# Performance work log

Measured on AMD Instinct MI355X. Metric: run time of the kernel, lower is better.

The kernel has to match this reference:

```python
import jax, jax.numpy as jnp
import numpy as np

NUM_GRAPHS = 1024  # static number of segments for global_mean_pool


def setup_inputs() -> dict:
    key = jax.random.key(0)
    ks = jax.random.split(key, 16)
    N, E, F_IN, H = 100000, 1000000, 32, 64
    NUM_ATOM, NUM_ACT, L = 16, 8, 3
    s = 0.05
    x = jax.random.normal(ks[0], (N, F_IN), dtype=jnp.float32)
    edge_index = jax.random.randint(ks[1], (2, E), 0, N, dtype=jnp.int64)
    batch = jnp.sort(jax.random.randint(ks[2], (N,), 0, NUM_GRAPHS, dtype=jnp.int64))
    W_emb = jax.random.normal(ks[3], (F_IN, H), dtype=jnp.float32) * s
    b_emb = jnp.zeros((H,), dtype=jnp.float32)
    W_convs = jax.random.normal(ks[4], (L, H, H), dtype=jnp.float32) * s
    b_convs = jnp.zeros((L, H), dtype=jnp.float32)
    W_act = jax.random.normal(ks[5], (H, NUM_ACT), dtype=jnp.float32) * s
    b_act = jnp.zeros((NUM_ACT,), dtype=jnp.float32)
    W_tgt = jax.random.normal(ks[6], (H, 1), dtype=jnp.float32) * s
    b_tgt = jnp.zeros((1,), dtype=jnp.float32)
    W_atom = jax.random.normal(ks[7], (H, NUM_ATOM), dtype=jnp.float32) * s
    b_atom = jnp.zeros((NUM_ATOM,), dtype=jnp.float32)
    return {"x": x, "edge_index": edge_index, "batch": batch,
            "W_emb": W_emb, "b_emb": b_emb, "W_convs": W_convs, "b_convs": b_convs,
            "W_act": W_act, "b_act": b_act, "W_tgt": W_tgt, "b_tgt": b_tgt,
            "W_atom": W_atom, "b_atom": b_atom}


def reference(x, edge_index, batch, W_emb, b_emb, W_convs, b_convs,
              W_act, b_act, W_tgt, b_tgt, W_atom, b_atom):
    N = x.shape[0]
    # --- GCN normalization with self-loops (PyG GCNConv default) ---
    self_idx = jnp.arange(N, dtype=edge_index.dtype)
    src = jnp.concatenate([edge_index[0], self_idx])  # message source (row)
    dst = jnp.concatenate([edge_index[1], self_idx])  # aggregation target (col)
    ones_e = jnp.ones(src.shape[0], dtype=x.dtype)
    deg = jax.ops.segment_sum(ones_e, dst, num_segments=N)  # in-degree + self-loop
    dinv = jnp.where(deg > 0, jax.lax.rsqrt(deg), 0.0)
    norm = (dinv[src] * dinv[dst])[:, None]  # [E+N, 1]

    h = jax.nn.relu(x @ W_emb + b_emb)  # node embedding
    for i in range(W_convs.shape[0]):
        m = (h @ W_convs[i])[src] * norm            # gather + scale
        agg = jax.ops.segment_sum(m, dst, num_segments=N)  # scatter-add
        h = jax.nn.relu(agg + b_convs[i])

    # --- global mean pool over graphs ---
    cnt = jax.ops.segment_sum(jnp.ones(N, dtype=x.dtype), batch, num_segments=NUM_GRAPHS)
    pooled = jax.ops.segment_sum(h, batch, num_segments=NUM_GRAPHS)
    pooled = pooled / jnp.maximum(cnt, 1.0)[:, None]

    action_type_logits = pooled @ W_act + b_act            # [G, num_action_types]
    target_node_logits = (h @ W_tgt + b_tgt)[:, 0]         # [N]
    new_atom_type_logits = pooled @ W_atom + b_atom        # [G, num_atom_types]
    return (action_type_logits, target_node_logits, new_atom_type_logits, h)
```

## Files before the change

kernel.cpp:

```cpp
#include <hip/hip_runtime.h>
#include <hip/hip_fp16.h>

#define HD 64
#define FIN 32
#define NG 1024
#define STRIDE 64
#define SLOT0 4
#define DEGCAP 59
#define SH 72

#define BINW 128
#define NBMAX 1024
#define EPB 8192
#define BINCAP 2048

typedef _Float16 f16x8 __attribute__((ext_vector_type(8)));
typedef float f32x4 __attribute__((ext_vector_type(4)));
typedef int i32x4 __attribute__((ext_vector_type(4)));

__device__ __forceinline__ int fmap(int jt, int c) {
    return (jt < 2) ? (2 * c + jt) : (32 + 2 * c + (jt - 2));
}

__global__ __launch_bounds__(256) void k_prep(const int* __restrict__ dst,
                                              int* __restrict__ blkHist,
                                              int E, int NBINS,
                                              __half2* __restrict__ BaZR,
                                              __half2* __restrict__ BbZR,
                                              const float* __restrict__ Wconv,
                                              __half* __restrict__ Wf, int wtotal,
                                              const float* __restrict__ Wemb,
                                              __half* __restrict__ Wef) {
    __shared__ int hist[NBMAX];
    int b = blockIdx.x, t = threadIdx.x;
    if (b < 48) {
        int tid = b * 256 + t;
        if (tid < wtotal) {
            int layer = tid >> 12;
            int r = tid & 4095;
            int frag = r >> 9, lane = (r >> 3) & 63, e = r & 7;
            int jt = frag >> 1, kh = frag & 1;
            int k = kh * 32 + (lane >> 4) * 8 + e;
            int n = fmap(jt, lane & 15);
            Wf[tid] = (_Float16)Wconv[(size_t)layer * 4096 + k * 64 + n];
        }
    } else if (b < 56) {
        int tid = (b - 48) * 256 + t;
        if (tid < 2048) {
            int jt = tid >> 9, lane = (tid >> 3) & 63, e = tid & 7;
            int k = (lane >> 4) * 8 + e;
            int n = fmap(jt, lane & 15);
            Wef[tid] = (_Float16)Wemb[k * HD + n];
        }
    } else if (b == 56) {
        __half2 z = __floats2half2_rn(0.f, 0.f);
        if (t < 32) BaZR[t] = z;
        else if (t < 64) BbZR[t - 32] = z;
    }
    int e0 = b * EPB;
    if (e0 < E) {
        for (int i = t; i < NBMAX; i += 256) hist[i] = 0;
        __syncthreads();
        int e1 = e0 + EPB; if (e1 > E) e1 = E;
        for (int e = e0 + t; e < e1; e += 256) atomicAdd(&hist[dst[e] >> 7], 1);
        __syncthreads();
        for (int i = t; i < NBINS; i += 256) blkHist[b * NBMAX + i] = hist[i];
    }
}

__global__ __launch_bounds__(256) void k_scanA(int* __restrict__ blkHist,
                                               int* __restrict__ binTot, int nb) {
    __shared__ int s[256];
    int i = blockIdx.x;
    int t = threadIdx.x;
    int x = (t < nb) ? blkHist[t * NBMAX + i] : 0;
    s[t] = x;
    __syncthreads();
    for (int off = 1; off < 256; off <<= 1) {
        int v = s[t];
        int u = (t >= off) ? s[t - off] : 0;
        __syncthreads();
        s[t] = v + u;
        __syncthreads();
    }
    if (t < nb) blkHist[t * NBMAX + i] = s[t] - x;
    if (t == 255) binTot[i] = s[255];
}

__global__ __launch_bounds__(256) void k_scatter(const int* __restrict__ src,
                                                 const int* __restrict__ dst,
                                                 const int* __restrict__ blkBase,
                                                 int* __restrict__ binned,
                                                 int E, int NBINS) {
    __shared__ int base[NBMAX];
    __shared__ int lpos[NBMAX];
    int b = blockIdx.x, t = threadIdx.x;
    for (int i = t; i < NBMAX; i += 256) {
        lpos[i] = 0;
        base[i] = (i < NBINS) ? blkBase[b * NBMAX + i] : 0;
    }
    __syncthreads();
    int e0 = b * EPB;
    int e1 = e0 + EPB; if (e1 > E) e1 = E;
    for (int e = e0 + t; e < e1; e += 256) {
        int d = dst[e];
        int bin = d >> 7;
        int off = base[bin] + atomicAdd(&lpos[bin], 1);
        if (off < BINCAP)
            binned[bin * BINCAP + off] = (src[e] << 7) | (d & (BINW - 1));
    }
}

__global__ __launch_bounds__(256) void k_csr(const int* __restrict__ binned,
                                             const int* __restrict__ binTot,
                                             int* __restrict__ col, int N) {
    __shared__ int img[BINW * 64];
    __shared__ int cnt[BINW];
    int b = blockIdx.x, t = threadIdx.x;
    for (int i = t; i < BINW; i += 256) cnt[i] = 0;
    __syncthreads();
    int s = b * BINCAP;
    int tot = binTot[b]; if (tot > BINCAP) tot = BINCAP;
    int e = s + tot;
    for (int i = s + t; i < e; i += 256) {
        int w = binned[i];
        int ld = w & (BINW - 1);
        int p = atomicAdd(&cnt[ld], 1);
        if (p < STRIDE - SLOT0) img[ld * 64 + SLOT0 + p] = (int)((unsigned)w >> 7);
    }
    __syncthreads();
    for (int i = t; i < BINW; i += 256) img[i * 64] = cnt[i];
    __syncthreads();
    int v0 = b * BINW;
    int* out = col + ((size_t)v0 << 6);
    for (int j = t; j < BINW * 16; j += 256) {
        int row = j >> 4, j16 = j & 15;
        int node = v0 + row;
        int deg = cnt[row]; if (deg > DEGCAP) deg = DEGCAP;
        bool keep = (j16 == 0) || (j16 <= ((deg + 3) >> 2));
        if (node < N && keep) {
            i32x4 val = *(i32x4*)&img[j * 4];
            __builtin_nontemporal_store(val, (i32x4*)(out + j * 4));
        }
    }
}

__device__ __forceinline__ void gemm_from_lds(const __half* hs, const float* dvs,
                                              const float4* __restrict__ Wf4,
                                              __half2* __restrict__ Bout,
                                              int node0, int N, int t) {
    int lane = t & 63;
    int wv = t >> 6;
    int lm = lane & 15, kq = lane >> 4;
    union U { float4 f; f16x8 h; };
    U a0, a1;
    const __half* hrow = hs + (size_t)(wv * 16 + lm) * SH;
    a0.f = *(const float4*)(hrow + kq * 8);
    a1.f = *(const float4*)(hrow + 32 + kq * 8);
    f32x4 acc[4];
#pragma unroll
    for (int jt = 0; jt < 4; jt++) acc[jt] = (f32x4){0.f, 0.f, 0.f, 0.f};
#pragma unroll
    for (int jt = 0; jt < 4; jt++) {
        U b0, b1;
        b0.f = Wf4[(jt * 2 + 0) * 64 + lane];
        b1.f = Wf4[(jt * 2 + 1) * 64 + lane];
        acc[jt] = __builtin_amdgcn_mfma_f32_16x16x32_f16(a0.h, b0.h, acc[jt], 0, 0, 0);
        acc[jt] = __builtin_amdgcn_mfma_f32_16x16x32_f16(a1.h, b1.h, acc[jt], 0, 0, 0);
    }
#pragma unroll
    for (int r = 0; r < 4; r++) {
        int lv = wv * 16 + kq * 4 + r;
        int v = node0 + lv;
        if (v < N) {
            float dv = dvs[lv];
            *(Bout + (size_t)v * 32 + lm) = __floats2half2_rn(acc[0][r] * dv, acc[1][r] * dv);
            *(Bout + (size_t)v * 32 + 16 + lm) = __floats2half2_rn(acc[2][r] * dv, acc[3][r] * dv);
        }
    }
}

__global__ __launch_bounds__(256) void k_emb_gemm0(const float* __restrict__ x,
                                                   const float4* __restrict__ Wef4,
                                                   const float* __restrict__ bemb,
                                                   const int* __restrict__ col,
                                                   const float4* __restrict__ Wf0,
                                                   __half2* __restrict__ Bout, int N) {
    __shared__ __half hs[64 * SH];
    __shared__ float dvs[64];
    int t = threadIdx.x;
    int lane = t & 63;
    int wv = t >> 6;
    int node0 = blockIdx.x * 64;
    int nodew = node0 + wv * 16;
    int m = lane & 15, kq = lane >> 4;

    int vm = nodew + m;
    if (vm > N - 1) vm = N - 1;
    const float4* xr = (const float4*)(x + (size_t)vm * FIN + kq * 8);
    float4 xa = xr[0], xb = xr[1];
    f16x8 a;
    a[0] = (_Float16)xa.x; a[1] = (_Float16)xa.y; a[2] = (_Float16)xa.z; a[3] = (_Float16)xa.w;
    a[4] = (_Float16)xb.x; a[5] = (_Float16)xb.y; a[6] = (_Float16)xb.z; a[7] = (_Float16)xb.w;

    union U { float4 f; f16x8 h; };
    f32x4 acc[4];
#pragma unroll
    for (int jt = 0; jt < 4; jt++) {
        U b; b.f = Wef4[jt * 64 + lane];
        acc[jt] = (f32x4){0.f, 0.f, 0.f, 0.f};
        acc[jt] = __builtin_amdgcn_mfma_f32_16x16x32_f16(a, b.h, acc[jt], 0, 0, 0);
    }
    float b01x = bemb[2 * m], b01y = bemb[2 * m + 1];
    float b23x = bemb[32 + 2 * m], b23y = bemb[32 + 2 * m + 1];
    __half2 z = __floats2half2_rn(0.f, 0.f);
#pragma unroll
    for (int r = 0; r < 4; r++) {
        int lv = wv * 16 + kq * 4 + r;
        int v = node0 + lv;
        __half2 p01 = z, p23 = z;
        if (v < N) {
            p01 = __floats2half2_rn(fmaxf(acc[0][r] + b01x, 0.f),
                                    fmaxf(acc[1][r] + b01y, 0.f));
            p23 = __floats2half2_rn(fmaxf(acc[2][r] + b23x, 0.f),
                                    fmaxf(acc[3][r] + b23y, 0.f));
        }
        *(__half2*)(hs + (size_t)lv * SH + 2 * m) = p01;
        *(__half2*)(hs + (size_t)lv * SH + 32 + 2 * m) = p23;
        if (m == 0)
            dvs[lv] = (v < N) ? rsqrtf((float)(col[(size_t)v << 6] + 1)) : 1.f;
    }
    __syncthreads();
    gemm_from_lds(hs, dvs, Wf0, Bout, node0, N, t);
}

__global__ __launch_bounds__(256) void k_layer(const __half2* __restrict__ Bin,
                                               const int* __restrict__ col,
                                               const float* __restrict__ bias,
                                               const float4* __restrict__ Wnext,
                                               __half2* __restrict__ Bout,
                                               int N, int ZR) {
    __shared__ __half hs[64 * SH];
    __shared__ float dvs[64];
    int t = threadIdx.x;
    int lane = t & 63;
    int wv = t >> 6;
    int node0 = blockIdx.x * 64;
    int q = lane >> 4, p = lane & 15;
    float4 b4 = *(const float4*)(bias + 4 * p);

#pragma unroll
    for (int pass = 0; pass < 4; pass++) {
        int lv = wv * 16 + pass * 4 + q;
        int v = node0 + lv;
        int vc = (v < N) ? v : 0;
        const int* bucket = col + ((size_t)vc << 6);
        int degraw = bucket[0];
        int deg = degraw > DEGCAP ? DEGCAP : degraw;
        int dmax = deg;
        dmax = max(dmax, __shfl_xor(dmax, 16, 64));
        dmax = max(dmax, __shfl_xor(dmax, 32, 64));
        int rounds = (dmax + 4) >> 2;

        float2 a0 = make_float2(0.f, 0.f), a1 = make_float2(0.f, 0.f);
        for (int rd = 0; rd < rounds; rd++) {
            int4 iq = *(const int4*)(bucket + SLOT0 + rd * 4);
            int idx[4] = {iq.x, iq.y, iq.z, iq.w};
#pragma unroll
            for (int r = 0; r < 4; r++) {
                int i = rd * 4 + r;
                idx[r] = (i < deg) ? idx[r] : ((i == deg) ? vc : ZR);
            }
            float2 raw[4];
#pragma unroll
            for (int r = 0; r < 4; r++)
                raw[r] = *(const float2*)(Bin + (size_t)idx[r] * 32 + p * 2);
#pragma unroll
            for (int r = 0; r < 4; r++) {
                float2 f0 = __half22float2(((const __half2*)&raw[r])[0]);
                float2 f1 = __half22float2(((const __half2*)&raw[r])[1]);
                a0.x += f0.x; a0.y += f0.y; a1.x += f1.x; a1.y += f1.y;
            }
        }
        float dv = rsqrtf((float)(degraw + 1));
        float r0 = fmaxf(dv * a0.x + b4.x, 0.f);
        float r1 = fmaxf(dv * a0.y + b4.y, 0.f);
        float r2 = fmaxf(dv * a1.x + b4.z, 0.f);
        float r3 = fmaxf(dv * a1.y + b4.w, 0.f);
        if (v >= N) { r0 = r1 = r2 = r3 = 0.f; dv = 1.f; }
        __half* hrow = hs + (size_t)lv * SH + 4 * p;
        *(__half2*)(hrow) = __floats2half2_rn(r0, r1);
        *(__half2*)(hrow + 2) = __floats2half2_rn(r2, r3);
        if (p == 0) dvs[lv] = dv;
    }
    __syncthreads();
    gemm_from_lds(hs, dvs, Wnext, Bout, node0, N, t);
}

__global__ __launch_bounds__(256) void k_gather_last(const __half2* __restrict__ Bin,
                                                     const int* __restrict__ col,
                                                     const float* __restrict__ bias,
                                                     float* __restrict__ hout,
                                                     const float* __restrict__ Wtgt,
                                                     const float* __restrict__ btgt,
                                                     float* __restrict__ tgt,
                                                     int N, int ZR) {
    int t = threadIdx.x;
    int lane = t & 63;
    int wv = t >> 6;
    int q = lane >> 4, p = lane & 15;
    int v = blockIdx.x * 16 + wv * 4 + q;
    if (v >= N) return;

    const int* bucket = col + ((size_t)v << 6);
    int degraw = bucket[0];
    int deg = degraw > DEGCAP ? DEGCAP : degraw;
    int dmax = deg;
    dmax = max(dmax, __shfl_xor(dmax, 16, 64));
    dmax = max(dmax, __shfl_xor(dmax, 32, 64));
    int rounds = (dmax + 4) >> 2;

    float2 a0 = make_float2(0.f, 0.f), a1 = make_float2(0.f, 0.f);
    for (int rd = 0; rd < rounds; rd++) {
        int4 iq = *(const int4*)(bucket + SLOT0 + rd * 4);
        int idx[4] = {iq.x, iq.y, iq.z, iq.w};
#pragma unroll
        for (int r = 0; r < 4; r++) {
            int i = rd * 4 + r;
            idx[r] = (i < deg) ? idx[r] : ((i == deg) ? v : ZR);
        }
        float2 raw[4];
#pragma unroll
        for (int r = 0; r < 4; r++)
            raw[r] = *(const float2*)(Bin + (size_t)idx[r] * 32 + p * 2);
#pragma unroll
        for (int r = 0; r < 4; r++) {
            float2 f0 = __half22float2(((const __half2*)&raw[r])[0]);
            float2 f1 = __half22float2(((const __half2*)&raw[r])[1]);
            a0.x += f0.x; a0.y += f0.y; a1.x += f1.x; a1.y += f1.y;
        }
    }
    float dv = rsqrtf((float)(degraw + 1));
    float4 b4 = *(const float4*)(bias + 4 * p);
    float r0 = fmaxf(dv * a0.x + b4.x, 0.f);
    float r1 = fmaxf(dv * a0.y + b4.y, 0.f);
    float r2 = fmaxf(dv * a1.x + b4.z, 0.f);
    float r3 = fmaxf(dv * a1.y + b4.w, 0.f);
    f32x4 o = (f32x4){r0, r1, r2, r3};
    __builtin_nontemporal_store(o, (f32x4*)(hout + (size_t)v * HD + 4 * p));
    float4 w4 = *(const float4*)(Wtgt + 4 * p);
    float pp = r0 * w4.x + r1 * w4.y + r2 * w4.z + r3 * w4.w;
    pp += __shfl_xor(pp, 1, 64); pp += __shfl_xor(pp, 2, 64);
    pp += __shfl_xor(pp, 4, 64); pp += __shfl_xor(pp, 8, 64);
    if (p == 0) __builtin_nontemporal_store(pp + btgt[0], tgt + v);
}

__global__ __launch_bounds__(256) void k_pool(const float* __restrict__ h,
                                              const int* __restrict__ batch,
                                              const float* __restrict__ Wact,
                                              const float* __restrict__ bact,
                                              const float* __restrict__ Watom,
                                              const float* __restrict__ batom,
                                              float* __restrict__ out_act,
                                              float* __restrict__ out_atom, int N) {
    int g = blockIdx.x;
    int t = threadIdx.x;
    int q = t >> 4, p = t & 15;
    int lo = 0, hi = N;
    while (lo < hi) { int mid = (lo + hi) >> 1; if (batch[mid] < g) lo = mid + 1; else hi = mid; }
    int s = lo;
    hi = N;
    while (lo < hi) { int mid = (lo + hi) >> 1; if (batch[mid] < g + 1) lo = mid + 1; else hi = mid; }
    int e2 = lo;
    float4 acc = make_float4(0.f, 0.f, 0.f, 0.f);
    for (int v = s + q; v < e2; v += 16) {
        float4 c = *(const float4*)(h + (size_t)v * HD + p * 4);
        acc.x += c.x; acc.y += c.y; acc.z += c.z; acc.w += c.w;
    }
    __shared__ float4 part[16][16];
    part[q][p] = acc;
    __syncthreads();
    __shared__ float pl[HD];
    if (t < 16) {
        float4 tot = part[0][t];
#pragma unroll
        for (int k = 1; k < 16; k++) {
            float4 c = part[k][t];
            tot.x += c.x; tot.y += c.y; tot.z += c.z; tot.w += c.w;
        }
        float cnt = fmaxf((float)(e2 - s), 1.f);
        pl[t * 4 + 0] = tot.x / cnt; pl[t * 4 + 1] = tot.y / cnt;
        pl[t * 4 + 2] = tot.z / cnt; pl[t * 4 + 3] = tot.w / cnt;
    }
    __syncthreads();
    if (t < 8) {
        float a = bact[t];
#pragma unroll
        for (int k = 0; k < HD; k++) a += pl[k] * Wact[k * 8 + t];
        out_act[g * 8 + t] = a;
    }
    if (t < 16) {
        float a = batom[t];
#pragma unroll
        for (int k = 0; k < HD; k++) a += pl[k] * Watom[k * 16 + t];
        out_atom[g * 16 + t] = a;
    }
}

extern "C" void kernel_launch(void* const* d_in, const int* in_sizes, int n_in,
                              void* d_out, int out_size, void* d_ws, size_t ws_size,
                              hipStream_t stream) {
    const float* x     = (const float*)d_in[0];
    const int*   ei    = (const int*)d_in[1];
    const int*   batch = (const int*)d_in[2];
    const float* Wemb  = (const float*)d_in[3];
    const float* bemb  = (const float*)d_in[4];
    const float* Wconv = (const float*)d_in[5];
    const float* bconv = (const float*)d_in[6];
    const float* Wact  = (const float*)d_in[7];
    const float* bact  = (const float*)d_in[8];
    const float* Wtgt  = (const float*)d_in[9];
    const float* btgt  = (const float*)d_in[10];
    const float* Watom = (const float*)d_in[11];
    const float* batom = (const float*)d_in[12];

    const int N = in_sizes[0] / FIN;
    const int E = in_sizes[1] / 2;
    const int L = in_sizes[5] / (HD * HD);
    const int Npad = (N + 63) & ~63;
    const int ZR = Npad;

    int*     col = (int*)d_ws;
    __half2* Ba  = (__half2*)(col + ((size_t)N << 6));
    __half2* Bb  = Ba + (size_t)(Npad + 64) * 32;
    __half*  Wf  = (__half*)(Bb + (size_t)(Npad + 64) * 32);
    __half*  Wef = Wf + (size_t)L * 4096;

    int* binned  = (int*)Bb;
    int* blkHist = (int*)((char*)Bb + (8u << 20));
    int* binTot  = (int*)((char*)Bb + (9u << 20));

    const int* srcA = ei;
    const int* dstA = ei + E;

    float* out_act  = (float*)d_out;
    float* out_tgt  = out_act + (size_t)NG * 8;
    float* out_atom = out_tgt + N;
    float* out_h    = out_atom + (size_t)NG * 16;

    const int nbG = (N + 63) / 64;
    const int nbLast = (N + 15) / 16;
    const int wtotal = L * 4096;
    const int nbF1 = (E + EPB - 1) / EPB;
    const int NBINS = (N + BINW - 1) / BINW;
    const int nbPrep = nbF1 > 57 ? nbF1 : 57;

    k_prep<<<nbPrep, 256, 0, stream>>>(dstA, blkHist, E, NBINS,
                                       Ba + (size_t)ZR * 32, Bb + (size_t)ZR * 32,
                                       Wconv, Wf, wtotal, Wemb, Wef);
    k_scanA<<<NBINS, 256, 0, stream>>>(blkHist, binTot, nbF1);
    k_scatter<<<nbF1, 256, 0, stream>>>(srcA, dstA, blkHist, binned, E, NBINS);
    k_csr<<<NBINS, 256, 0, stream>>>(binned, binTot, col, N);
    k_emb_gemm0<<<nbG, 256, 0, stream>>>(x, (const float4*)Wef, bemb, col,
                                         (const float4*)Wf, Ba, N);

    __half2* cur = Ba;
    __half2* nxt = Bb;
    for (int l = 0; l < L - 1; ++l) {
        k_layer<<<nbG, 256, 0, stream>>>(cur, col, bconv + l * HD,
                                         (const float4*)(Wf + (size_t)(l + 1) * 4096),
                                         nxt, N, ZR);
        __half2* tmp = cur; cur = nxt; nxt = tmp;
    }
    k_gather_last<<<nbLast, 256, 0, stream>>>(cur, col, bconv + (size_t)(L - 1) * HD,
                                              out_h, Wtgt, btgt, out_tgt, N, ZR);
    k_pool<<<NG, 256, 0, stream>>>(out_h, batch, Wact, bact, Watom, batom,
                                   out_act, out_atom, N);
}
```

Before: 233.8 us.

## Drop the scan kernel by computing bin prefix sums inside scatter and csr

Removes the separate k_scanA launch. k_prep now writes the per-block histogram transposed, k_scatter computes each bin's base offset by summing earlier blocks serially, and k_csr gets each bin total with a shared atomic reduction. This saves one kernel launch and dependency point, at the cost of a serial prefix loop of up to ~123 reads per bin per thread in scatter. It also replaces nontemporal stores with plain stores for the CSR column output and the final h output, which changes how those writes interact with the cache.

Measured after the change: 256.6 us. 1.1x slower.

```diff
diff --git a/kernel.cpp b/kernel.cpp
--- a/kernel.cpp
+++ b/kernel.cpp
@@ -23,7 +23,7 @@
 }
 
 __global__ __launch_bounds__(256) void k_prep(const int* __restrict__ dst,
-                                              int* __restrict__ blkHist,
+                                              int* __restrict__ blkHistT,
                                               int E, int NBINS,
                                               __half2* __restrict__ BaZR,
                                               __half2* __restrict__ BbZR,
@@ -64,32 +64,13 @@
         int e1 = e0 + EPB; if (e1 > E) e1 = E;
         for (int e = e0 + t; e < e1; e += 256) atomicAdd(&hist[dst[e] >> 7], 1);
         __syncthreads();
-        for (int i = t; i < NBINS; i += 256) blkHist[b * NBMAX + i] = hist[i];
-    }
-}
-
-__global__ __launch_bounds__(256) void k_scanA(int* __restrict__ blkHist,
-                                               int* __restrict__ binTot, int nb) {
-    __shared__ int s[256];
-    int i = blockIdx.x;
-    int t = threadIdx.x;
-    int x = (t < nb) ? blkHist[t * NBMAX + i] : 0;
-    s[t] = x;
-    __syncthreads();
-    for (int off = 1; off < 256; off <<= 1) {
-        int v = s[t];
-        int u = (t >= off) ? s[t - off] : 0;
-        __syncthreads();
-        s[t] = v + u;
-        __syncthreads();
-    }
-    if (t < nb) blkHist[t * NBMAX + i] = s[t] - x;
-    if (t == 255) binTot[i] = s[255];
+        for (int i = t; i < NBINS; i += 256) blkHistT[i * 256 + b] = hist[i];
+    }
 }
 
 __global__ __launch_bounds__(256) void k_scatter(const int* __restrict__ src,
                                                  const int* __restrict__ dst,
-                                                 const int* __restrict__ blkBase,
+                                                 const int* __restrict__ blkHistT,
                                                  int* __restrict__ binned,
                                                  int E, int NBINS) {
     __shared__ int base[NBMAX];
@@ -97,7 +78,12 @@
     int b = blockIdx.x, t = threadIdx.x;
     for (int i = t; i < NBMAX; i += 256) {
         lpos[i] = 0;
-        base[i] = (i < NBINS) ? blkBase[b * NBMAX + i] : 0;
+        int s = 0;
+        if (i < NBINS) {
+            const int* row = blkHistT + i * 256;
+            for (int b2 = 0; b2 < b; b2++) s += row[b2];
+        }
+        base[i] = s;
     }
     __syncthreads();
     int e0 = b * EPB;
@@ -112,15 +98,19 @@
 }
 
 __global__ __launch_bounds__(256) void k_csr(const int* __restrict__ binned,
-                                             const int* __restrict__ binTot,
+                                             const int* __restrict__ blkHistT, int nb,
                                              int* __restrict__ col, int N) {
     __shared__ int img[BINW * 64];
     __shared__ int cnt[BINW];
+    __shared__ int stot;
     int b = blockIdx.x, t = threadIdx.x;
     for (int i = t; i < BINW; i += 256) cnt[i] = 0;
-    __syncthreads();
+    if (t == 0) stot = 0;
+    __syncthreads();
+    if (t < nb) atomicAdd(&stot, blkHistT[b * 256 + t]);
+    __syncthreads();
+    int tot = stot; if (tot > BINCAP) tot = BINCAP;
     int s = b * BINCAP;
-    int tot = binTot[b]; if (tot > BINCAP) tot = BINCAP;
     int e = s + tot;
     for (int i = s + t; i < e; i += 256) {
         int w = binned[i];
@@ -138,10 +128,8 @@
         int node = v0 + row;
         int deg = cnt[row]; if (deg > DEGCAP) deg = DEGCAP;
         bool keep = (j16 == 0) || (j16 <= ((deg + 3) >> 2));
-        if (node < N && keep) {
-            i32x4 val = *(i32x4*)&img[j * 4];
-            __builtin_nontemporal_store(val, (i32x4*)(out + j * 4));
-        }
+        if (node < N && keep)
+            *(i32x4*)(out + j * 4) = *(i32x4*)&img[j * 4];
     }
 }
 
@@ -346,8 +334,7 @@
     float r1 = fmaxf(dv * a0.y + b4.y, 0.f);
     float r2 = fmaxf(dv * a1.x + b4.z, 0.f);
     float r3 = fmaxf(dv * a1.y + b4.w, 0.f);
-    f32x4 o = (f32x4){r0, r1, r2, r3};
-    __builtin_nontemporal_store(o, (f32x4*)(hout + (size_t)v * HD + 4 * p));
+    *(f32x4*)(hout + (size_t)v * HD + 4 * p) = (f32x4){r0, r1, r2, r3};
     float4 w4 = *(const float4*)(Wtgt + 4 * p);
     float pp = r0 * w4.x + r1 * w4.y + r2 * w4.z + r3 * w4.w;
     pp += __shfl_xor(pp, 1, 64); pp += __shfl_xor(pp, 2, 64);
@@ -436,9 +423,8 @@
     __half*  Wf  = (__half*)(Bb + (size_t)(Npad + 64) * 32);
     __half*  Wef = Wf + (size_t)L * 4096;
 
-    int* binned  = (int*)Bb;
-    int* blkHist = (int*)((char*)Bb + (8u << 20));
-    int* binTot  = (int*)((char*)Bb + (9u << 20));
+    int* binned   = (int*)Bb;
+    int* blkHistT = (int*)((char*)Bb + (8u << 20));
 
     const int* srcA = ei;
     const int* dstA = ei + E;
@@ -455,12 +441,11 @@
     const int NBINS = (N + BINW - 1) / BINW;
     const int nbPrep = nbF1 > 57 ? nbF1 : 57;
 
-    k_prep<<<nbPrep, 256, 0, stream>>>(dstA, blkHist, E, NBINS,
+    k_prep<<<nbPrep, 256, 0, stream>>>(dstA, blkHistT, E, NBINS,
                                        Ba + (size_t)ZR * 32, Bb + (size_t)ZR * 32,
                                        Wconv, Wf, wtotal, Wemb, Wef);
-    k_scanA<<<NBINS, 256, 0, stream>>>(blkHist, binTot, nbF1);
-    k_scatter<<<nbF1, 256, 0, stream>>>(srcA, dstA, blkHist, binned, E, NBINS);
-    k_csr<<<NBINS, 256, 0, stream>>>(binned, binTot, col, N);
+    k_scatter<<<nbF1, 256, 0, stream>>>(srcA, dstA, blkHistT, binned, E, NBINS);
+    k_csr<<<NBINS, 256, 0, stream>>>(binned, blkHistT, nbF1, col, N);
     k_emb_gemm0<<<nbG, 256, 0, stream>>>(x, (const float4*)Wef, bemb, col,
                                          (const float4*)Wf, Ba, N);
 
```
